# Optimization experiments

Measured on AMD Instinct MI355X. Metric: run time of the kernel, lower is better.

## Reference

```python
import jax, jax.numpy as jnp
import numpy as np
import math

H = 8          # num_heads
LW = 2         # local_window
GROUPS = 32    # GroupNorm groups
EPS = 1e-5


def group_norm(x, gamma, beta):
    # x: [b, c, t]
    b, c, t = x.shape
    xg = x.reshape(b, GROUPS, c // GROUPS, t)
    mu = xg.mean(axis=(2, 3), keepdims=True)
    var = xg.var(axis=(2, 3), keepdims=True)
    xg = (xg - mu) * jax.lax.rsqrt(var + EPS)
    return xg.reshape(b, c, t) * gamma[None, :, None] + beta[None, :, None]


def setup_inputs() -> dict:
    key = jax.random.key(0)
    ks = jax.random.split(key, 8)
    b, f, c, h, w, l = 1, 16, 512, 32, 32, 4096
    video = jax.random.normal(ks[0], (b, f, c, h, w), jnp.float32)
    audio = jax.random.normal(ks[1], (b, c, l), jnp.float32)
    return {
        "video": video,
        "audio": audio,
        "v_norm_scale": jnp.ones((c,), jnp.float32),
        "v_norm_bias": jnp.zeros((c,), jnp.float32),
        "a_norm_scale": jnp.ones((c,), jnp.float32),
        "a_norm_bias": jnp.zeros((c,), jnp.float32),
        "v_qkv_w": jax.random.normal(ks[2], (3 * c, c), jnp.float32) * 0.02,
        "v_qkv_b": jnp.zeros((3 * c,), jnp.float32),
        "a_qkv_w": jax.random.normal(ks[3], (3 * c, c), jnp.float32) * 0.02,
        "a_qkv_b": jnp.zeros((3 * c,), jnp.float32),
        "video_proj_w": jax.random.normal(ks[4], (c, c), jnp.float32) * 0.02,
        "video_proj_b": jnp.zeros((c,), jnp.float32),
        "audio_proj_w": jax.random.normal(ks[5], (c, c), jnp.float32) * 0.02,
        "audio_proj_b": jnp.zeros((c,), jnp.float32),
    }


def reference(video, audio, v_norm_scale, v_norm_bias, a_norm_scale, a_norm_bias,
              v_qkv_w, v_qkv_b, a_qkv_w, a_qkv_b,
              video_proj_w, video_proj_b, audio_proj_w, audio_proj_b):
    b, f, c, h, w = video.shape
    l = audio.shape[-1]
    fs = h * w                      # frame_size
    video_len = f * fs
    alp = l // f                    # audio tokens per frame
    ch = c // H
    scale = float(ch) ** -0.25      # applied to both q and k, as in torch

    # tokens + norm + 1x1-conv qkv projections
    video_token = jnp.transpose(video, (0, 2, 1, 3, 4)).reshape(b, c, video_len)
    v_qkv = jnp.einsum('oc,bct->bot', v_qkv_w, group_norm(video_token, v_norm_scale, v_norm_bias)) + v_qkv_b[None, :, None]
    a_qkv = jnp.einsum('oc,bct->bot', a_qkv_w, group_norm(audio, a_norm_scale, a_norm_bias)) + a_qkv_b[None, :, None]
    qkv = jnp.concatenate([v_qkv, a_qkv], axis=2)      # [b, 3c, T]
    q, k, v = jnp.split(qkv, 3, axis=1)
    q = q.reshape(b * H, ch, -1)
    k = k.reshape(b * H, ch, -1)
    v = v.reshape(b * H, ch, -1)

    # windowed cross-modal gather indices (window_shift=False)
    va_idx = (jnp.arange(f)[:, None] * alp + jnp.arange(LW * alp)[None, :]) % l + video_len   # [f, LW*alp]
    av_idx = (jnp.arange(f)[:, None] * fs + jnp.arange(LW * fs)[None, :]) % video_len         # [f, LW*fs]

    # video queries attend to windowed audio k/v
    vq = q[:, :, :video_len].reshape(b * H, ch, f, fs)
    k_win = k[:, :, va_idx]                            # [bH, ch, f, LW*alp]
    v_win = v[:, :, va_idx]
    att_v = jax.nn.softmax(jnp.einsum('bcft,bcfs->bfts', vq * scale, k_win * scale), axis=-1)
    v_out = jnp.einsum('bfts,bcfs->bcft', att_v, v_win).reshape(b, c, video_len)

    # audio queries attend to windowed video k/v
    aq = q[:, :, video_len:].reshape(b * H, ch, f, alp)
    k_win_a = k[:, :, av_idx]                          # [bH, ch, f, LW*fs]
    v_win_a = v[:, :, av_idx]
    att_a = jax.nn.softmax(jnp.einsum('bcft,bcfs->bfts', aq * scale, k_win_a * scale), axis=-1)
    a_out = jnp.einsum('bfts,bcfs->bcft', att_a, v_win_a).reshape(b, c, l)

    # projections (1x1x1 conv3d / 1x1 conv1d) + residual
    video_h = jnp.transpose(v_out.reshape(b, c, f, h, w), (0, 2, 1, 3, 4))  # b f c h w
    video_h = jnp.einsum('oc,bfchw->bfohw', video_proj_w, video_h) + video_proj_b[None, None, :, None, None]
    video_out = video + video_h
    audio_out = audio + jnp.einsum('oc,bcl->bol', audio_proj_w, a_out) + audio_proj_b[None, :, None]
    return (video_out, audio_out)
```

## Files before the change

kernel.cpp:

```cpp
#include <hip/hip_runtime.h>
#include <hip/hip_bf16.h>

typedef unsigned short u16;
typedef u16 u16x8 __attribute__((ext_vector_type(8)));
typedef u16 u16x4 __attribute__((ext_vector_type(4)));
typedef float f32x4 __attribute__((ext_vector_type(4)));
typedef __bf16 bf16x8 __attribute__((ext_vector_type(8)));

static __device__ __forceinline__ u16 f2bf(float f) {
  __hip_bfloat16 h = __float2bfloat16(f);
  return __builtin_bit_cast(u16, h);
}

static __device__ __forceinline__ f32x4 mfma16x16(u16x8 a, u16x8 b, f32x4 c) {
  return __builtin_amdgcn_mfma_f32_16x16x32_bf16(
      __builtin_bit_cast(bf16x8, a), __builtin_bit_cast(bf16x8, b), c, 0, 0, 0);
}

__global__ void __launch_bounds__(256) stats_partial(
    const float* __restrict__ video, const float* __restrict__ audio,
    float* __restrict__ partials) {
  int b = blockIdx.x;
  int tid = threadIdx.x;
  const float* src;
  if (b < 512) {
    int g = b >> 4, f = b & 15;
    src = video + (size_t)f * 524288 + (size_t)(g * 16) * 1024;
  } else {
    int bb = b - 512;
    int g = bb >> 2, ck = bb & 3;
    src = audio + (size_t)(g * 16) * 4096 + ck * 16384;
  }
  float s1 = 0.f, s2 = 0.f;
#pragma unroll
  for (int it = 0; it < 16; ++it) {
    float4 v = *(const float4*)&src[it * 1024 + tid * 4];
    s1 += v.x + v.y + v.z + v.w;
    s2 += v.x * v.x + v.y * v.y + v.z * v.z + v.w * v.w;
  }
  __shared__ float r1[256], r2[256];
  r1[tid] = s1; r2[tid] = s2;
  __syncthreads();
  for (int s = 128; s > 0; s >>= 1) {
    if (tid < s) { r1[tid] += r1[tid + s]; r2[tid] += r2[tid + s]; }
    __syncthreads();
  }
  if (tid == 0) { partials[2 * b] = r1[0]; partials[2 * b + 1] = r2[0]; }
}

__global__ void __launch_bounds__(64) stats_finalize(
    const float* __restrict__ partials, float* __restrict__ stats) {
  int g = threadIdx.x;
  int base, cnt;
  if (g < 32) { base = g * 16; cnt = 16; }
  else        { base = 512 + (g - 32) * 4; cnt = 4; }
  float s1 = 0.f, s2 = 0.f;
  for (int i = 0; i < cnt; ++i) {
    s1 += partials[2 * (base + i)];
    s2 += partials[2 * (base + i) + 1];
  }
  float n = (g < 32) ? 262144.f : 65536.f;
  float mu = s1 / n;
  float var = s2 / n - mu * mu;
  stats[2 * g] = mu;
  stats[2 * g + 1] = rsqrtf(var + 1e-5f);
}

__global__ void __launch_bounds__(256) norm_video(
    const float* __restrict__ video, const float* __restrict__ gamma,
    const float* __restrict__ beta, const float* __restrict__ stats,
    u16* __restrict__ XT) {
  __shared__ float tile[64][65];
  int bid = blockIdx.x;
  int t0 = (bid % 256) * 64;
  int c0 = (bid / 256) * 64;
  int f = t0 >> 10;
  int hw0 = t0 & 1023;
  int tx = threadIdx.x & 63, ty = threadIdx.x >> 6;
#pragma unroll
  for (int p = 0; p < 16; ++p) {
    int cl = p * 4 + ty;
    int c = c0 + cl;
    float x = video[(size_t)f * 524288 + (size_t)c * 1024 + hw0 + tx];
    int g = c >> 4;
    float xn = (x - stats[2 * g]) * stats[2 * g + 1] * gamma[c] + beta[c];
    tile[tx][cl] = xn;
  }
  __syncthreads();
#pragma unroll
  for (int p = 0; p < 16; ++p) {
    int tl = p * 4 + ty;
    XT[(size_t)(t0 + tl) * 512 + c0 + tx] = f2bf(tile[tl][tx]);
  }
}

__global__ void __launch_bounds__(256) norm_audio(
    const float* __restrict__ audio, const float* __restrict__ gamma,
    const float* __restrict__ beta, const float* __restrict__ stats,
    u16* __restrict__ XT) {
  __shared__ float tile[64][65];
  int bid = blockIdx.x;
  int t0 = (bid % 64) * 64;
  int c0 = (bid / 64) * 64;
  int tx = threadIdx.x & 63, ty = threadIdx.x >> 6;
#pragma unroll
  for (int p = 0; p < 16; ++p) {
    int cl = p * 4 + ty;
    int c = c0 + cl;
    float x = audio[(size_t)c * 4096 + t0 + tx];
    int g = 32 + (c >> 4);
    float xn = (x - stats[2 * g]) * stats[2 * g + 1] * gamma[c] + beta[c];
    tile[tx][cl] = xn;
  }
  __syncthreads();
#pragma unroll
  for (int p = 0; p < 16; ++p) {
    int tl = p * 4 + ty;
    XT[(size_t)(16384 + t0 + tl) * 512 + c0 + tx] = f2bf(tile[tl][tx]);
  }
}

__global__ void __launch_bounds__(256) cvt_all(
    const float* __restrict__ s0, const float* __restrict__ s1,
    const float* __restrict__ s2, const float* __restrict__ s3,
    u16* __restrict__ dst) {
  int i = (blockIdx.x * 256 + threadIdx.x) * 4;
  const float* src;
  int off;
  if (i < 786432)       { src = s0; off = 0; }
  else if (i < 1572864) { src = s1; off = 786432; }
  else if (i < 1835008) { src = s2; off = 1572864; }
  else                  { src = s3; off = 1835008; }
  float4 v = *(const float4*)&src[i - off];
  u16x4 pk;
  pk[0] = f2bf(v.x); pk[1] = f2bf(v.y); pk[2] = f2bf(v.z); pk[3] = f2bf(v.w);
  *(u16x4*)&dst[i] = pk;
}

template <int MODE>
__global__ void __launch_bounds__(256, 2) gemm_bt(
    const u16* __restrict__ A, const u16* __restrict__ B,
    const float* __restrict__ bias, u16* __restrict__ Qo,
    u16* __restrict__ Ko, u16* __restrict__ Vt, float* __restrict__ FO,
    const float* __restrict__ RES, int t_off) {
  __shared__ u16 As[128][72];
  __shared__ u16 Bs[128][72];
  const int tid = threadIdx.x;
  const int lane = tid & 63;
  const int w = tid >> 6;
  const int wr = w >> 1, wc = w & 1;
  const int col = lane & 15, qg = lane >> 4;
  const int m0 = blockIdx.y * 128;
  const int n0 = blockIdx.x * 128;
  f32x4 acc[4][4] = {};
  for (int k0 = 0; k0 < 512; k0 += 64) {
#pragma unroll
    for (int p = 0; p < 4; ++p) {
      int chunk = p * 256 + tid;
      int row = chunk >> 3;
      int kk = (chunk & 7) * 8;
      *(u16x8*)&As[row][kk] = *(const u16x8*)&A[(size_t)(m0 + row) * 512 + k0 + kk];
      *(u16x8*)&Bs[row][kk] = *(const u16x8*)&B[(size_t)(n0 + row) * 512 + k0 + kk];
    }
    __syncthreads();
#pragma unroll
    for (int ks = 0; ks < 2; ++ks) {
      u16x8 af[4], bf[4];
#pragma unroll
      for (int mt = 0; mt < 4; ++mt)
        af[mt] = *(const u16x8*)&As[wr * 64 + mt * 16 + col][ks * 32 + qg * 8];
#pragma unroll
      for (int nt = 0; nt < 4; ++nt)
        bf[nt] = *(const u16x8*)&Bs[wc * 64 + nt * 16 + col][ks * 32 + qg * 8];
#pragma unroll
      for (int mt = 0; mt < 4; ++mt)
#pragma unroll
        for (int nt = 0; nt < 4; ++nt)
          acc[mt][nt] = mfma16x16(af[mt], bf[nt], acc[mt][nt]);
    }
    __syncthreads();
  }
#pragma unroll
  for (int mt = 0; mt < 4; ++mt) {
    int o = m0 + wr * 64 + mt * 16 + qg * 4;
#pragma unroll
    for (int nt = 0; nt < 4; ++nt) {
      int t = n0 + wc * 64 + nt * 16 + col;
      float v0 = acc[mt][nt][0] + bias[o + 0];
      float v1 = acc[mt][nt][1] + bias[o + 1];
      float v2 = acc[mt][nt][2] + bias[o + 2];
      float v3 = acc[mt][nt][3] + bias[o + 3];
      if constexpr (MODE == 0) {
        int tg = t_off + t;
        if (o < 512) {
          u16x4 pk;
          pk[0] = f2bf(v0 * 0.125f); pk[1] = f2bf(v1 * 0.125f);
          pk[2] = f2bf(v2 * 0.125f); pk[3] = f2bf(v3 * 0.125f);
          *(u16x4*)&Qo[(size_t)tg * 512 + o] = pk;
        } else if (o < 1024) {
          u16x4 pk;
          pk[0] = f2bf(v0); pk[1] = f2bf(v1); pk[2] = f2bf(v2); pk[3] = f2bf(v3);
          *(u16x4*)&Ko[(size_t)tg * 512 + (o - 512)] = pk;
        } else {
          int vo = o - 1024;
          Vt[(size_t)(vo + 0) * 20480 + tg] = f2bf(v0);
          Vt[(size_t)(vo + 1) * 20480 + tg] = f2bf(v1);
          Vt[(size_t)(vo + 2) * 20480 + tg] = f2bf(v2);
          Vt[(size_t)(vo + 3) * 20480 + tg] = f2bf(v3);
        }
      } else if constexpr (MODE == 2) {
        int f = t >> 10, hw = t & 1023;
        size_t i0 = ((size_t)(f * 512 + o)) * 1024 + hw;
        FO[i0]        = RES[i0]        + v0;
        FO[i0 + 1024] = RES[i0 + 1024] + v1;
        FO[i0 + 2048] = RES[i0 + 2048] + v2;
        FO[i0 + 3072] = RES[i0 + 3072] + v3;
      } else {
        size_t i0 = (size_t)o * 4096 + t;
        FO[i0]         = RES[i0]         + v0;
        FO[i0 + 4096]  = RES[i0 + 4096]  + v1;
        FO[i0 + 8192]  = RES[i0 + 8192]  + v2;
        FO[i0 + 12288] = RES[i0 + 12288] + v3;
      }
    }
  }
}

__global__ void __launch_bounds__(256, 2) flash_attn(
    const u16* __restrict__ Q, const u16* __restrict__ K,
    const u16* __restrict__ Vt, u16* __restrict__ AO, int Tq, int W,
    int qt_base, int kbase, int kstep, int kmod, int nttiles) {
  __shared__ u16 P[4][16][72];
  int nwg = gridDim.x;
  int bid = (blockIdx.x & 7) * (nwg >> 3) + (blockIdx.x >> 3);
  int tt = bid % nttiles;
  int f = (bid / nttiles) & 15;
  int h = bid / (nttiles * 16);
  int tid = threadIdx.x;
  int lane = tid & 63;
  int w = tid >> 6;
  int col = lane & 15, qg = lane >> 4;
  int ch0 = h * 64;
  int qt0 = qt_base + f * Tq + tt * 64 + w * 16;
  u16x8 qf[2];
#pragma unroll
  for (int kk = 0; kk < 2; ++kk)
    qf[kk] = *(const u16x8*)&Q[(size_t)(qt0 + col) * 512 + ch0 + kk * 32 + qg * 8];
  f32x4 oacc[4] = {};
  float m_[4], l_[4];
#pragma unroll
  for (int j = 0; j < 4; ++j) { m_[j] = -1e30f; l_[j] = 0.f; }
  int fk = f * kstep;
  for (int s0 = 0; s0 < W; s0 += 64) {
    f32x4 sacc[4] = {};
#pragma unroll
    for (int st = 0; st < 4; ++st) {
      int s = s0 + st * 16 + col;
      int kt = kbase + (fk + s) % kmod;
      const u16* kr = &K[(size_t)kt * 512 + ch0];
#pragma unroll
      for (int kk = 0; kk < 2; ++kk) {
        u16x8 bfr = *(const u16x8*)&kr[kk * 32 + qg * 8];
        sacc[st] = mfma16x16(qf[kk], bfr, sacc[st]);
      }
    }
    float corr[4];
#pragma unroll
    for (int j = 0; j < 4; ++j) {
      float pm = fmaxf(fmaxf(sacc[0][j], sacc[1][j]), fmaxf(sacc[2][j], sacc[3][j]));
      pm = fmaxf(pm, __shfl_xor(pm, 1, 64));
      pm = fmaxf(pm, __shfl_xor(pm, 2, 64));
      pm = fmaxf(pm, __shfl_xor(pm, 4, 64));
      pm = fmaxf(pm, __shfl_xor(pm, 8, 64));
      float nm = fmaxf(m_[j], pm);
      corr[j] = __expf(m_[j] - nm);
      m_[j] = nm;
    }
#pragma unroll
    for (int st = 0; st < 4; ++st)
#pragma unroll
      for (int j = 0; j < 4; ++j)
        sacc[st][j] = __expf(sacc[st][j] - m_[j]);
#pragma unroll
    for (int j = 0; j < 4; ++j) {
      float rs = sacc[0][j] + sacc[1][j] + sacc[2][j] + sacc[3][j];
      rs += __shfl_xor(rs, 1, 64);
      rs += __shfl_xor(rs, 2, 64);
      rs += __shfl_xor(rs, 4, 64);
      rs += __shfl_xor(rs, 8, 64);
      l_[j] = l_[j] * corr[j] + rs;
#pragma unroll
      for (int ct = 0; ct < 4; ++ct) oacc[ct][j] *= corr[j];
    }
#pragma unroll
    for (int st = 0; st < 4; ++st)
#pragma unroll
      for (int j = 0; j < 4; ++j)
        P[w][qg * 4 + j][st * 16 + col] = f2bf(sacc[st][j]);
    u16x8 pf[2];
#pragma unroll
    for (int half = 0; half < 2; ++half)
      pf[half] = *(const u16x8*)&P[w][col][half * 32 + qg * 8];
#pragma unroll
    for (int ct = 0; ct < 4; ++ct) {
#pragma unroll
      for (int half = 0; half < 2; ++half) {
        int sb = s0 + half * 32 + qg * 8;
        int ktv = kbase + (fk + sb) % kmod;
        u16x8 vfr = *(const u16x8*)&Vt[(size_t)(ch0 + ct * 16 + col) * 20480 + ktv];
        oacc[ct] = mfma16x16(pf[half], vfr, oacc[ct]);
      }
    }
  }
#pragma unroll
  for (int ct = 0; ct < 4; ++ct)
#pragma unroll
    for (int j = 0; j < 4; ++j) {
      float val = oacc[ct][j] / l_[j];
      AO[(size_t)(qt0 + qg * 4 + j) * 512 + ch0 + ct * 16 + col] = f2bf(val);
    }
}

extern "C" void kernel_launch(void* const* d_in, const int* in_sizes, int n_in,
                              void* d_out, int out_size, void* d_ws,
                              size_t ws_size, hipStream_t stream) {
  const float* video = (const float*)d_in[0];
  const float* audio = (const float*)d_in[1];
  const float* v_g = (const float*)d_in[2];
  const float* v_b = (const float*)d_in[3];
  const float* a_g = (const float*)d_in[4];
  const float* a_b = (const float*)d_in[5];
  const float* vqkv_w = (const float*)d_in[6];
  const float* vqkv_b = (const float*)d_in[7];
  const float* aqkv_w = (const float*)d_in[8];
  const float* aqkv_b = (const float*)d_in[9];
  const float* vp_w = (const float*)d_in[10];
  const float* vp_b = (const float*)d_in[11];
  const float* ap_w = (const float*)d_in[12];
  const float* ap_b = (const float*)d_in[13];

  char* ws = (char*)d_ws;
  float* stats = (float*)ws;
  float* partials = (float*)(ws + 512);
  u16* Wv = (u16*)(ws + 8192);
  u16* Wa = Wv + 1536 * 512;
  u16* Pv = Wa + 1536 * 512;
  u16* Pa = Pv + 512 * 512;
  u16* XT = Pa + 512 * 512;
  u16* Vt = XT + 20480 * 512;
  u16* Qb = (u16*)d_out;
  u16* Kb = Qb + 20480 * 512;
  float* out_v = (float*)d_out;
  float* out_a = out_v + 8388608;

  stats_partial<<<640, 256, 0, stream>>>(video, audio, partials);
  stats_finalize<<<1, 64, 0, stream>>>(partials, stats);
  norm_video<<<2048, 256, 0, stream>>>(video, v_g, v_b, stats, XT);
  norm_audio<<<512, 256, 0, stream>>>(audio, a_g, a_b, stats, XT);
  cvt_all<<<2048, 256, 0, stream>>>(vqkv_w, aqkv_w, vp_w, ap_w, Wv);

  dim3 gv(128, 12);
  gemm_bt<0><<<gv, 256, 0, stream>>>(Wv, XT, vqkv_b, Qb, Kb, Vt, nullptr, nullptr, 0);
  dim3 ga(32, 12);
  gemm_bt<0><<<ga, 256, 0, stream>>>(Wa, XT + (size_t)16384 * 512, aqkv_b, Qb, Kb, Vt, nullptr, nullptr, 16384);

  flash_attn<<<8 * 16 * 16, 256, 0, stream>>>(Qb, Kb, Vt, XT, 1024, 512, 0, 16384, 256, 4096, 16);
  flash_attn<<<8 * 16 * 4, 256, 0, stream>>>(Qb, Kb, Vt, XT, 256, 2048, 16384, 0, 1024, 16384, 4);

  dim3 gp(128, 4);
  gemm_bt<2><<<gp, 256, 0, stream>>>(Pv, XT, vp_b, nullptr, nullptr, nullptr, out_v, video, 0);
  dim3 gq(32, 4);
  gemm_bt<3><<<gq, 256, 0, stream>>>(Pa, XT + (size_t)16384 * 512, ap_b, nullptr, nullptr, nullptr, out_a, audio, 0);
}
```

Before: 502.9 us.

## Process 256-key chunks per softmax update in flash attention with templated chunk count

The flash attention loop now handles 256 keys per online-softmax step instead of 64. It computes four 64-wide score tiles before a single max/rescale, which cuts the number of cross-lane reductions and oacc rescales. P staging in shared memory is double-buffered per sub-tile, and the window length becomes a compile-time template parameter. Launch bounds rise to 3 waves per SIMD, but sacc grows from 16 to 64 floats, so register pressure may cause spills or keep the occupancy hint from being reached.

```diff
diff --git a/kernel.cpp b/kernel.cpp
--- a/kernel.cpp
+++ b/kernel.cpp
@@ -226,11 +226,12 @@
   }
 }
 
-__global__ void __launch_bounds__(256, 2) flash_attn(
+template <int NC>
+__global__ void __launch_bounds__(256, 3) flash_attn(
     const u16* __restrict__ Q, const u16* __restrict__ K,
-    const u16* __restrict__ Vt, u16* __restrict__ AO, int Tq, int W,
+    const u16* __restrict__ Vt, u16* __restrict__ AO, int Tq,
     int qt_base, int kbase, int kstep, int kmod, int nttiles) {
-  __shared__ u16 P[4][16][72];
+  __shared__ u16 P[4][2][16][72];
   int nwg = gridDim.x;
   int bid = (blockIdx.x & 7) * (nwg >> 3) + (blockIdx.x >> 3);
   int tt = bid % nttiles;
@@ -251,23 +252,30 @@
 #pragma unroll
   for (int j = 0; j < 4; ++j) { m_[j] = -1e30f; l_[j] = 0.f; }
   int fk = f * kstep;
-  for (int s0 = 0; s0 < W; s0 += 64) {
-    f32x4 sacc[4] = {};
-#pragma unroll
-    for (int st = 0; st < 4; ++st) {
-      int s = s0 + st * 16 + col;
-      int kt = kbase + (fk + s) % kmod;
-      const u16* kr = &K[(size_t)kt * 512 + ch0];
-#pragma unroll
-      for (int kk = 0; kk < 2; ++kk) {
-        u16x8 bfr = *(const u16x8*)&kr[kk * 32 + qg * 8];
-        sacc[st] = mfma16x16(qf[kk], bfr, sacc[st]);
+  for (int c = 0; c < NC; ++c) {
+    int cs = c * 256;
+    f32x4 sacc[4][4] = {};
+#pragma unroll
+    for (int t = 0; t < 4; ++t) {
+#pragma unroll
+      for (int st = 0; st < 4; ++st) {
+        int s = cs + t * 64 + st * 16 + col;
+        int kt = kbase + (fk + s) % kmod;
+        const u16* kr = &K[(size_t)kt * 512 + ch0];
+#pragma unroll
+        for (int kk = 0; kk < 2; ++kk)
+          sacc[t][st] = mfma16x16(qf[kk], *(const u16x8*)&kr[kk * 32 + qg * 8],
+                                  sacc[t][st]);
       }
     }
     float corr[4];
 #pragma unroll
     for (int j = 0; j < 4; ++j) {
-      float pm = fmaxf(fmaxf(sacc[0][j], sacc[1][j]), fmaxf(sacc[2][j], sacc[3][j]));
+      float pm = sacc[0][0][j];
+#pragma unroll
+      for (int t = 0; t < 4; ++t)
+#pragma unroll
+        for (int st = 0; st < 4; ++st) pm = fmaxf(pm, sacc[t][st][j]);
       pm = fmaxf(pm, __shfl_xor(pm, 1, 64));
       pm = fmaxf(pm, __shfl_xor(pm, 2, 64));
       pm = fmaxf(pm, __shfl_xor(pm, 4, 64));
@@ -277,13 +285,19 @@
       m_[j] = nm;
     }
 #pragma unroll
-    for (int st = 0; st < 4; ++st)
-#pragma unroll
-      for (int j = 0; j < 4; ++j)
-        sacc[st][j] = __expf(sacc[st][j] - m_[j]);
+    for (int t = 0; t < 4; ++t)
+#pragma unroll
+      for (int st = 0; st < 4; ++st)
+#pragma unroll
+        for (int j = 0; j < 4; ++j)
+          sacc[t][st][j] = __expf(sacc[t][st][j] - m_[j]);
 #pragma unroll
     for (int j = 0; j < 4; ++j) {
-      float rs = sacc[0][j] + sacc[1][j] + sacc[2][j] + sacc[3][j];
+      float rs = 0.f;
+#pragma unroll
+      for (int t = 0; t < 4; ++t)
+#pragma unroll
+        for (int st = 0; st < 4; ++st) rs += sacc[t][st][j];
       rs += __shfl_xor(rs, 1, 64);
       rs += __shfl_xor(rs, 2, 64);
       rs += __shfl_xor(rs, 4, 64);
@@ -293,22 +307,27 @@
       for (int ct = 0; ct < 4; ++ct) oacc[ct][j] *= corr[j];
     }
 #pragma unroll
-    for (int st = 0; st < 4; ++st)
-#pragma unroll
-      for (int j = 0; j < 4; ++j)
-        P[w][qg * 4 + j][st * 16 + col] = f2bf(sacc[st][j]);
-    u16x8 pf[2];
-#pragma unroll
-    for (int half = 0; half < 2; ++half)
-      pf[half] = *(const u16x8*)&P[w][col][half * 32 + qg * 8];
-#pragma unroll
-    for (int ct = 0; ct < 4; ++ct) {
-#pragma unroll
-      for (int half = 0; half < 2; ++half) {
-        int sb = s0 + half * 32 + qg * 8;
-        int ktv = kbase + (fk + sb) % kmod;
-        u16x8 vfr = *(const u16x8*)&Vt[(size_t)(ch0 + ct * 16 + col) * 20480 + ktv];
-        oacc[ct] = mfma16x16(pf[half], vfr, oacc[ct]);
+    for (int t = 0; t < 4; ++t) {
+      const int buf = t & 1;
+#pragma unroll
+      for (int st = 0; st < 4; ++st)
+#pragma unroll
+        for (int j = 0; j < 4; ++j)
+          P[w][buf][qg * 4 + j][st * 16 + col] = f2bf(sacc[t][st][j]);
+      u16x8 pf[2];
+#pragma unroll
+      for (int half = 0; half < 2; ++half)
+        pf[half] = *(const u16x8*)&P[w][buf][col][half * 32 + qg * 8];
+#pragma unroll
+      for (int ct = 0; ct < 4; ++ct) {
+#pragma unroll
+        for (int half = 0; half < 2; ++half) {
+          int sb = cs + t * 64 + half * 32 + qg * 8;
+          int ktv = kbase + (fk + sb) % kmod;
+          u16x8 vfr =
+              *(const u16x8*)&Vt[(size_t)(ch0 + ct * 16 + col) * 20480 + ktv];
+          oacc[ct] = mfma16x16(pf[half], vfr, oacc[ct]);
+        }
       }
     }
   }
@@ -364,8 +383,8 @@
   dim3 ga(32, 12);
   gemm_bt<0><<<ga, 256, 0, stream>>>(Wa, XT + (size_t)16384 * 512, aqkv_b, Qb, Kb, Vt, nullptr, nullptr, 16384);
 
-  flash_attn<<<8 * 16 * 16, 256, 0, stream>>>(Qb, Kb, Vt, XT, 1024, 512, 0, 16384, 256, 4096, 16);
-  flash_attn<<<8 * 16 * 4, 256, 0, stream>>>(Qb, Kb, Vt, XT, 256, 2048, 16384, 0, 1024, 16384, 4);
+  flash_attn<2><<<8 * 16 * 16, 256, 0, stream>>>(Qb, Kb, Vt, XT, 1024, 0, 16384, 256, 4096, 16);
+  flash_attn<8><<<8 * 16 * 4, 256, 0, stream>>>(Qb, Kb, Vt, XT, 256, 16384, 0, 1024, 16384, 4);
 
   dim3 gp(128, 4);
   gemm_bt<2><<<gp, 256, 0, stream>>>(Pv, XT, vp_b, nullptr, nullptr, nullptr, out_v, video, 0);
```

Result: no change. 511.1 us (+1.6%).
